# Performance work log

Hardware: AMD Instinct MI355X
Metric: run time of the kernel (lower is better)

The kernel has to match this reference:

```python
import jax, jax.numpy as jnp
import numpy as np

N = 50000          # num nodes
E = 800000         # edges per adjacency (avg degree 16)
NFEAT = 512
NHID = 256
NCLS = 100
LN_EPS = 1e-5


def spmm(rows, cols, vals, feat):
    # sparse [N,N] @ dense [N,F] via gather + segment-sum scatter
    return jax.ops.segment_sum(vals[:, None] * feat[cols], rows, num_segments=N)


def layernorm(h, g, b):
    mu = jnp.mean(h, axis=-1, keepdims=True)
    var = jnp.var(h, axis=-1, keepdims=True)
    return (h - mu) * jax.lax.rsqrt(var + LN_EPS) * g + b


def setup_inputs() -> dict:
    key = jax.random.key(0)
    ks = jax.random.split(key, 20)
    inp = {
        "x": jax.random.normal(ks[0], (N, NFEAT), dtype=jnp.float32),
        "adj_rows": jax.random.randint(ks[1], (4, E), 0, N, dtype=jnp.int32),
        "adj_cols": jax.random.randint(ks[2], (4, E), 0, N, dtype=jnp.int32),
        "adj_vals": jax.random.uniform(ks[3], (4, E), dtype=jnp.float32) / 16.0,
    }
    def lin(k, fin, fout):
        s = 1.0 / np.sqrt(fin)
        kw, kb = jax.random.split(k)
        return (jax.random.uniform(kw, (fin, fout), minval=-s, maxval=s, dtype=jnp.float32),
                jax.random.uniform(kb, (fout,), minval=-s, maxval=s, dtype=jnp.float32))
    # layer 0: GraphSage(nfeat -> nhid), LayerNorm over 2*nhid
    inp["W0"], inp["b0"] = lin(ks[4], NFEAT, NHID)
    inp["ln0_g"] = jnp.ones((2 * NHID,), jnp.float32)
    inp["ln0_b"] = jnp.zeros((2 * NHID,), jnp.float32)
    # layer 1: GCN(2*nhid -> nhid)
    inp["W1"], inp["b1"] = lin(ks[5], 2 * NHID, NHID)
    # layer 2: GraphSage(nhid -> nhid), LayerNorm over 2*nhid
    inp["W2"], inp["b2"] = lin(ks[6], NHID, NHID)
    inp["ln2_g"] = jnp.ones((2 * NHID,), jnp.float32)
    inp["ln2_b"] = jnp.zeros((2 * NHID,), jnp.float32)
    # layer 3: GCN(2*nhid -> nhid)
    inp["W3"], inp["b3"] = lin(ks[7], 2 * NHID, NHID)
    # output linear (nhid -> num_classes)
    inp["Wout"], inp["bout"] = lin(ks[8], NHID, NCLS)
    return inp


def reference(x, adj_rows, adj_cols, adj_vals,
              W0, b0, ln0_g, ln0_b, W1, b1, W2, b2, ln2_g, ln2_b, W3, b3,
              Wout, bout):
    # layer 0: GraphSage — feat = Linear(x); h = LN(concat([feat, A@feat])); ReLU; dropout(p=0)=id
    feat = x @ W0 + b0
    agg = spmm(adj_rows[0], adj_cols[0], adj_vals[0], feat)
    h = jax.nn.relu(layernorm(jnp.concatenate([feat, agg], axis=1), ln0_g, ln0_b))
    # layer 1: GCN — h = A @ Linear(h); ReLU
    h = jax.nn.relu(spmm(adj_rows[1], adj_cols[1], adj_vals[1], h @ W1 + b1))
    # layer 2: GraphSage
    feat = h @ W2 + b2
    agg = spmm(adj_rows[2], adj_cols[2], adj_vals[2], feat)
    h = jax.nn.relu(layernorm(jnp.concatenate([feat, agg], axis=1), ln2_g, ln2_b))
    # layer 3: GCN
    h = jax.nn.relu(spmm(adj_rows[3], adj_cols[3], adj_vals[3], h @ W3 + b3))
    # output head
    return h @ Wout + bout
```

## Files before the change

### kernel.cpp

```cpp
#include <hip/hip_runtime.h>

#define N_NODES 50000
#define E_EDGES 800000
#define NFEAT   512
#define NHID    256
#define NCLS    100
#define LN_EPS  1e-5f

#define NB     196
#define CHUNKA 6144
#define CAPB   6656

typedef __attribute__((ext_vector_type(8))) short bf16x8;
typedef __attribute__((ext_vector_type(4))) float f32x4;

__device__ __forceinline__ ushort bf16_rne(float x) {
    unsigned u = __float_as_uint(x);
    unsigned r = u + 0x7FFFu + ((u >> 16) & 1u);
    return (ushort)(r >> 16);
}
__device__ __forceinline__ float bf16_to_f(ushort h) {
    return __uint_as_float(((unsigned)h) << 16);
}

__device__ __forceinline__ void gload16(const void* g, void* l) {
    __builtin_amdgcn_global_load_lds(
        (const __attribute__((address_space(1))) unsigned int*)g,
        (__attribute__((address_space(3))) unsigned int*)l, 16, 0, 0);
}

__global__ __launch_bounds__(256)
void wsplit_kernel(const float* __restrict__ W, ushort* __restrict__ WT,
                   int K, int Nc, int NP)
{
    const int idx = blockIdx.x * 256 + threadIdx.x;
    if (idx >= NP * K) return;
    const int n = idx / K, k = idx - n * K;
    const float w = (n < Nc) ? W[(size_t)k * Nc + n] : 0.f;
    WT[idx] = bf16_rne(w);
}

__global__ __launch_bounds__(256)
void xconv_kernel(const float* __restrict__ x, ushort* __restrict__ xb, int n8)
{
    const int idx = blockIdx.x * 256 + threadIdx.x;
    if (idx >= n8) return;
    const float4 v0 = ((const float4*)x)[idx * 2];
    const float4 v1 = ((const float4*)x)[idx * 2 + 1];
    bf16x8 h;
    h[0] = (short)bf16_rne(v0.x); h[1] = (short)bf16_rne(v0.y);
    h[2] = (short)bf16_rne(v0.z); h[3] = (short)bf16_rne(v0.w);
    h[4] = (short)bf16_rne(v1.x); h[5] = (short)bf16_rne(v1.y);
    h[6] = (short)bf16_rne(v1.z); h[7] = (short)bf16_rne(v1.w);
    *(bf16x8*)&xb[idx * 8] = h;
}

template<int WF32, int WBF>
__global__ __launch_bounds__(512)
void gemm_mfma_bf16(const ushort* __restrict__ A1, const ushort* __restrict__ A2,
                    int K1, int K, const ushort* __restrict__ BT,
                    const float* __restrict__ bias, float* __restrict__ C,
                    ushort* __restrict__ Cbf, int M, int Nc)
{
    __shared__ __align__(16) ushort Ah[2][128 * 32];
    __shared__ __align__(16) ushort Bh[2][128 * 32];

    const int tid = threadIdx.x;
    const int bm  = blockIdx.x * 128;
    const int bn  = blockIdx.y * 128;
    const int w   = tid >> 6;
    const int l   = tid & 63;
    const int wm  = (w >> 2) * 64;
    const int wn  = (w & 3) * 32;
    const int fr  = l & 15;
    const int fq  = l >> 4;

    const int gro = l >> 2;
    const int gch = ((l & 3) ^ (gro & 3)) * 8;
    const int ldsbase = (16 * w) * 32;

    f32x4 acc[4][2];
    #pragma unroll
    for (int i = 0; i < 4; ++i) {
        acc[i][0] = (f32x4){0.f, 0.f, 0.f, 0.f};
        acc[i][1] = (f32x4){0.f, 0.f, 0.f, 0.f};
    }

    const int K2 = K - K1;
    const int NS = K / 32;

    auto stage = [&](int s, int b) {
        const int k0 = s * 32;
        gload16(&BT[(size_t)(bn + 16 * w + gro) * K + k0 + gch], &Bh[b][ldsbase]);
        const ushort* asrc;
        if (k0 < K1) asrc = &A1[(size_t)(bm + 16 * w + gro) * K1 + k0 + gch];
        else         asrc = &A2[(size_t)(bm + 16 * w + gro) * K2 + (k0 - K1) + gch];
        gload16(asrc, &Ah[b][ldsbase]);
    };

    stage(0, 0);
    __syncthreads();

    int cur = 0;
    for (int s = 0; s < NS; ++s) {
        if (s + 1 < NS) stage(s + 1, cur ^ 1);

        bf16x8 bf[2];
        #pragma unroll
        for (int nf = 0; nf < 2; ++nf) {
            const int r = wn + nf * 16 + fr;
            bf[nf] = *(const bf16x8*)&Bh[cur][r * 32 + ((fq ^ (r & 3)) * 8)];
        }
        #pragma unroll
        for (int mf = 0; mf < 4; ++mf) {
            const int r = wm + mf * 16 + fr;
            const bf16x8 af = *(const bf16x8*)&Ah[cur][r * 32 + ((fq ^ (r & 3)) * 8)];
            acc[mf][0] = __builtin_amdgcn_mfma_f32_16x16x32_bf16(af, bf[0], acc[mf][0], 0, 0, 0);
            acc[mf][1] = __builtin_amdgcn_mfma_f32_16x16x32_bf16(af, bf[1], acc[mf][1], 0, 0, 0);
        }
        __syncthreads();
        cur ^= 1;
    }

    #pragma unroll
    for (int mf = 0; mf < 4; ++mf) {
        #pragma unroll
        for (int r = 0; r < 4; ++r) {
            const int row = bm + wm + mf * 16 + fq * 4 + r;
            if (row >= M) continue;
            #pragma unroll
            for (int nf = 0; nf < 2; ++nf) {
                const int col = bn + wn + nf * 16 + fr;
                if (col < Nc) {
                    const float v = acc[mf][nf][r] + bias[col];
                    if (WF32) C[(size_t)row * Nc + col] = v;
                    if (WBF)  Cbf[(size_t)row * Nc + col] = bf16_rne(v);
                }
            }
        }
    }
}

__global__ __launch_bounds__(256)
void bin_kernel(const int* __restrict__ rows, const int* __restrict__ cols,
                const float* __restrict__ vals, int* __restrict__ bcur,
                int2* __restrict__ est)
{
    __shared__ int cnt[NB];
    __shared__ int scn[256];
    __shared__ int cstart[NB];
    __shared__ int ccur[NB];
    __shared__ int garr[NB];
    __shared__ __align__(16) int2 buf[CHUNKA];

    const int a  = blockIdx.y;
    const int e0 = blockIdx.x * CHUNKA;
    const int n  = min(CHUNKA, E_EDGES - e0);
    const int t  = threadIdx.x;
    const int*   rp = rows + (size_t)a * E_EDGES + e0;
    const int*   cp = cols + (size_t)a * E_EDGES + e0;
    const float* vp = vals + (size_t)a * E_EDGES + e0;

    if (t < NB) cnt[t] = 0;
    __syncthreads();
    for (int i = t; i < n; i += 256) atomicAdd(&cnt[((unsigned)rp[i]) >> 8], 1);
    __syncthreads();

    scn[t] = (t < NB) ? cnt[t] : 0;
    __syncthreads();
    for (int off = 1; off < 256; off <<= 1) {
        const int v = (t >= off) ? scn[t - off] : 0;
        __syncthreads();
        scn[t] += v;
        __syncthreads();
    }
    if (t < NB) {
        const int ex = scn[t] - cnt[t];
        cstart[t] = ex;
        ccur[t]   = ex;
        garr[t]   = atomicAdd(&bcur[a * NB + t], cnt[t]);
    }
    __syncthreads();

    for (int i = t; i < n; i += 256) {
        const unsigned r = (unsigned)rp[i];
        const int b = r >> 8;
        const int p = atomicAdd(&ccur[b], 1);
        buf[p] = make_int2((int)((r << 16) | (unsigned)cp[i]), __float_as_int(vp[i]));
    }
    __syncthreads();

    for (int i = t; i < n; i += 256) {
        const int2 en = buf[i];
        const int b = ((unsigned)en.x) >> 24;
        const int slot = garr[b] + (i - cstart[b]);
        if (slot < CAPB)
            est[((size_t)(a * NB + b)) * CAPB + slot] = en;
    }
}

__global__ __launch_bounds__(256)
void bscan_kernel(const int* __restrict__ bcur, int* __restrict__ bbase)
{
    __shared__ int s[256];
    const int a = blockIdx.x;
    const int t = threadIdx.x;
    const int v = (t < NB) ? bcur[a * NB + t] : 0;
    s[t] = v;
    __syncthreads();
    for (int off = 1; off < 256; off <<= 1) {
        const int u = (t >= off) ? s[t - off] : 0;
        __syncthreads();
        s[t] += u;
        __syncthreads();
    }
    if (t < NB) bbase[a * NB + t] = s[t] - v;
}

__global__ __launch_bounds__(256)
void sort_kernel(const int* __restrict__ bcur, const int* __restrict__ bbase,
                 const int2* __restrict__ est, int2* __restrict__ cpk,
                 int* __restrict__ rowstart)
{
    __shared__ __align__(16) int2 sbuf[CAPB];
    __shared__ __align__(16) int2 obuf[CAPB];
    __shared__ int cnt[256];
    __shared__ int scn[256];
    __shared__ int cur[256];

    const int a = blockIdx.y;
    const int b = blockIdx.x;
    const int t = threadIdx.x;
    const int nb = min(bcur[a * NB + b], CAPB);
    const size_t slots = ((size_t)(a * NB + b)) * CAPB;

    for (int i = t; i < nb; i += 256) sbuf[i] = est[slots + i];
    cnt[t] = 0;
    __syncthreads();
    for (int i = t; i < nb; i += 256)
        atomicAdd(&cnt[(((unsigned)sbuf[i].x) >> 16) & 255], 1);
    __syncthreads();

    scn[t] = cnt[t];
    __syncthreads();
    for (int off = 1; off < 256; off <<= 1) {
        const int v = (t >= off) ? scn[t - off] : 0;
        __syncthreads();
        scn[t] += v;
        __syncthreads();
    }
    const int excl = scn[t] - cnt[t];
    cur[t] = excl;

    const int bb = bbase[a * NB + b];
    const int r0 = b << 8;
    if (r0 + t < N_NODES)
        rowstart[(size_t)a * (N_NODES + 1) + r0 + t] = bb + excl;
    if (b == NB - 1 && t == 0)
        rowstart[(size_t)a * (N_NODES + 1) + N_NODES] = E_EDGES;
    __syncthreads();

    for (int i = t; i < nb; i += 256) {
        const int2 en = sbuf[i];
        const int r = (((unsigned)en.x) >> 16) & 255;
        const int p = atomicAdd(&cur[r], 1);
        obuf[p] = make_int2(en.x & 0xFFFF, en.y);
    }
    __syncthreads();

    int2* co = cpk + (size_t)a * E_EDGES + bb;
    for (int i = t; i < nb; i += 256) co[i] = obuf[i];
}

template<int LNFUSE>
__global__ __launch_bounds__(256)
void spmm_kernel(const int* __restrict__ rowstart, const int2* __restrict__ cpk,
                 const ushort* __restrict__ feat, ushort* __restrict__ out0,
                 ushort* __restrict__ out1, const float* __restrict__ g,
                 const float* __restrict__ be)
{
    const int row  = __builtin_amdgcn_readfirstlane((blockIdx.x * 256 + threadIdx.x) >> 6);
    const int lane = threadIdx.x & 63;

    const int s = __builtin_amdgcn_readfirstlane(rowstart[row]);
    const int e = __builtin_amdgcn_readfirstlane(rowstart[row + 1]);

    const ushort* fbase = feat + lane * 4;
    float ax = 0.f, ay = 0.f, az = 0.f, aw = 0.f;

    for (int j = s; j < e; j += 16) {
        #pragma unroll
        for (int q = 0; q < 16; ++q) {
            if (j + q < e) {
                const int2 ev = cpk[j + q];
                const float v = __int_as_float(ev.y);
                const uint2 f = *(const uint2*)(fbase + (size_t)ev.x * NHID);
                ax += v * __uint_as_float(f.x << 16);
                ay += v * __uint_as_float(f.x & 0xFFFF0000u);
                az += v * __uint_as_float(f.y << 16);
                aw += v * __uint_as_float(f.y & 0xFFFF0000u);
            }
        }
    }

    if (LNFUSE) {
        const uint2 fx = *(const uint2*)(fbase + (size_t)row * NHID);
        float xf[4] = {__uint_as_float(fx.x << 16), __uint_as_float(fx.x & 0xFFFF0000u),
                       __uint_as_float(fx.y << 16), __uint_as_float(fx.y & 0xFFFF0000u)};

        float sum = xf[0] + xf[1] + xf[2] + xf[3] + ax + ay + az + aw;
        #pragma unroll
        for (int m = 1; m < 64; m <<= 1) sum += __shfl_xor(sum, m, 64);
        const float mean = sum * (1.f / 512.f);

        float sq = 0.f;
        #pragma unroll
        for (int jj = 0; jj < 4; ++jj) { const float d = xf[jj] - mean; sq += d * d; }
        { float d; d = ax - mean; sq += d * d; d = ay - mean; sq += d * d;
          d = az - mean; sq += d * d; d = aw - mean; sq += d * d; }
        #pragma unroll
        for (int m = 1; m < 64; m <<= 1) sq += __shfl_xor(sq, m, 64);
        const float rstd = rsqrtf(sq * (1.f / 512.f) + LN_EPS);

        const int col = lane * 4;
        const float av[4] = {ax, ay, az, aw};
        ushort4 o0, o1;
        float t0[4], t1[4];
        #pragma unroll
        for (int jj = 0; jj < 4; ++jj) {
            t0[jj] = fmaxf((xf[jj] - mean) * rstd * g[col + jj] + be[col + jj], 0.f);
            t1[jj] = fmaxf((av[jj] - mean) * rstd * g[256 + col + jj] + be[256 + col + jj], 0.f);
        }
        o0.x = bf16_rne(t0[0]); o0.y = bf16_rne(t0[1]); o0.z = bf16_rne(t0[2]); o0.w = bf16_rne(t0[3]);
        o1.x = bf16_rne(t1[0]); o1.y = bf16_rne(t1[1]); o1.z = bf16_rne(t1[2]); o1.w = bf16_rne(t1[3]);
        *(ushort4*)&out0[(size_t)row * NHID + col] = o0;
        *(ushort4*)&out1[(size_t)row * NHID + col] = o1;
    } else {
        ushort4 o;
        o.x = bf16_rne(fmaxf(ax, 0.f)); o.y = bf16_rne(fmaxf(ay, 0.f));
        o.z = bf16_rne(fmaxf(az, 0.f)); o.w = bf16_rne(fmaxf(aw, 0.f));
        *(ushort4*)&out0[(size_t)row * NHID + lane * 4] = o;
    }
}

extern "C" void kernel_launch(void* const* d_in, const int* in_sizes, int n_in,
                              void* d_out, int out_size, void* d_ws, size_t ws_size,
                              hipStream_t stream)
{
    const float* x    = (const float*)d_in[0];
    const int*   rows = (const int*)  d_in[1];
    const int*   cols = (const int*)  d_in[2];
    const float* vals = (const float*)d_in[3];
    const float* W0   = (const float*)d_in[4];
    const float* b0   = (const float*)d_in[5];
    const float* g0   = (const float*)d_in[6];
    const float* be0  = (const float*)d_in[7];
    const float* W1   = (const float*)d_in[8];
    const float* b1   = (const float*)d_in[9];
    const float* W2   = (const float*)d_in[10];
    const float* b2   = (const float*)d_in[11];
    const float* g2   = (const float*)d_in[12];
    const float* be2  = (const float*)d_in[13];
    const float* W3   = (const float*)d_in[14];
    const float* b3   = (const float*)d_in[15];
    const float* Wout = (const float*)d_in[16];
    const float* bout = (const float*)d_in[17];
    float* out = (float*)d_out;

    char* wsb = (char*)d_ws;
    size_t off = 0;
    auto carve = [&](size_t bytes) { void* p = wsb + off; off += (bytes + 255) & ~(size_t)255; return p; };
    int*    rowstart = (int*)   carve((size_t)4 * (N_NODES + 1) * 4);
    int*    bcur     = (int*)   carve((size_t)4 * NB * 4);
    int*    bbase    = (int*)   carve((size_t)4 * NB * 4);
    int2*   cpk      = (int2*)  carve((size_t)4 * E_EDGES * 8);
    int2*   est      = (int2*)  carve((size_t)4 * NB * CAPB * 8);
    ushort* Xb       = (ushort*)carve((size_t)N_NODES * NFEAT * 2);
    ushort* F        = (ushort*)carve((size_t)N_NODES * NHID * 2);
    ushort* P        = (ushort*)carve((size_t)N_NODES * NHID * 2);
    ushort* Q        = (ushort*)carve((size_t)N_NODES * NHID * 2);
    ushort* G        = (ushort*)carve((size_t)N_NODES * NHID * 2);
    ushort* H        = (ushort*)carve((size_t)N_NODES * NHID * 2);
    ushort* W0T = (ushort*)carve((size_t)256 * 512 * 2);
    ushort* W1T = (ushort*)carve((size_t)256 * 512 * 2);
    ushort* W2T = (ushort*)carve((size_t)256 * 256 * 2);
    ushort* W3T = (ushort*)carve((size_t)256 * 512 * 2);
    ushort* WoT = (ushort*)carve((size_t)128 * 256 * 2);
    carve(131072);

    const dim3 blk(256);
    const dim3 blkg(512);
    const dim3 g_gemm(391, 2);
    const dim3 g_head(391, 1);
    const dim3 g_bin((E_EDGES + CHUNKA - 1) / CHUNKA, 4);
    const dim3 g_sort(NB, 4);
    const int  row_blocks = (N_NODES * 64 + 255) / 256;

    wsplit_kernel<<<(256*512 + 255)/256, blk, 0, stream>>>(W0,   W0T, 512, 256, 256);
    wsplit_kernel<<<(256*512 + 255)/256, blk, 0, stream>>>(W1,   W1T, 512, 256, 256);
    wsplit_kernel<<<(256*256 + 255)/256, blk, 0, stream>>>(W2,   W2T, 256, 256, 256);
    wsplit_kernel<<<(256*512 + 255)/256, blk, 0, stream>>>(W3,   W3T, 512, 256, 256);
    wsplit_kernel<<<(128*256 + 255)/256, blk, 0, stream>>>(Wout, WoT, 256, 100, 128);
    xconv_kernel<<<(N_NODES * NFEAT / 8 + 255)/256, blk, 0, stream>>>(x, Xb, N_NODES * NFEAT / 8);

    hipMemsetAsync(bcur, 0, (size_t)4 * NB * 4, stream);
    bin_kernel<<<g_bin, blk, 0, stream>>>(rows, cols, vals, bcur, est);
    bscan_kernel<<<4, blk, 0, stream>>>(bcur, bbase);
    sort_kernel<<<g_sort, blk, 0, stream>>>(bcur, bbase, est, cpk, rowstart);

    const int* rs0 = rowstart;
    const int* rs1 = rowstart + (N_NODES + 1);
    const int* rs2 = rowstart + 2 * (N_NODES + 1);
    const int* rs3 = rowstart + 3 * (N_NODES + 1);
    const int2* c0 = cpk;
    const int2* c1 = cpk + E_EDGES;
    const int2* c2 = cpk + 2 * (size_t)E_EDGES;
    const int2* c3 = cpk + 3 * (size_t)E_EDGES;

    gemm_mfma_bf16<0,1><<<g_gemm, blkg, 0, stream>>>(Xb, Xb, 512, 512, W0T, b0, nullptr, F, N_NODES, 256);
    spmm_kernel<1><<<row_blocks, blk, 0, stream>>>(rs0, c0, F, P, Q, g0, be0);

    gemm_mfma_bf16<0,1><<<g_gemm, blkg, 0, stream>>>(P, Q, 256, 512, W1T, b1, nullptr, G, N_NODES, 256);
    spmm_kernel<0><<<row_blocks, blk, 0, stream>>>(rs1, c1, G, H, nullptr, nullptr, nullptr);

    gemm_mfma_bf16<0,1><<<g_gemm, blkg, 0, stream>>>(H, H, 256, 256, W2T, b2, nullptr, F, N_NODES, 256);
    spmm_kernel<1><<<row_blocks, blk, 0, stream>>>(rs2, c2, F, P, Q, g2, be2);

    gemm_mfma_bf16<0,1><<<g_gemm, blkg, 0, stream>>>(P, Q, 256, 512, W3T, b3, nullptr, G, N_NODES, 256);
    spmm_kernel<0><<<row_blocks, blk, 0, stream>>>(rs3, c3, G, H, nullptr, nullptr, nullptr);

    gemm_mfma_bf16<1,0><<<g_head, blkg, 0, stream>>>(H, H, 256, 256, WoT, bout, out, nullptr, N_NODES, 100);
}
```

Before: 529.1 us.

## Merge prep kernels and memset, fold bucket scan into sort, split SpMM tail

The five weight-transpose launches, the x-to-bf16 conversion and the bucket-counter memset are merged into one prep kernel. The separate bucket prefix-scan kernel is removed; each sort block now computes its own base offset with a shared-memory reduction over the preceding bucket counts. The SpMM inner loop drops the per-edge bounds check by running full 16-edge groups unguarded, followed by a scalar remainder loop. This cuts about eight launches and some branch overhead, at the cost of redundant per-block reductions in the sort kernel.

Result: faster. 484.5 us (-8.4%).

```diff
diff --git a/kernel.cpp b/kernel.cpp
--- a/kernel.cpp
+++ b/kernel.cpp
@@ -11,6 +11,10 @@
 #define CHUNKA 6144
 #define CAPB   6656
 
+#define WT_TOTAL  (256*512 + 256*512 + 256*256 + 256*512 + 128*256)
+#define XC_TOTAL  (N_NODES * NFEAT / 8)
+#define PREP_TOTAL (WT_TOTAL + XC_TOTAL + 4 * NB)
+
 typedef __attribute__((ext_vector_type(8))) short bf16x8;
 typedef __attribute__((ext_vector_type(4))) float f32x4;
 
@@ -30,29 +34,40 @@
 }
 
 __global__ __launch_bounds__(256)
-void wsplit_kernel(const float* __restrict__ W, ushort* __restrict__ WT,
-                   int K, int Nc, int NP)
-{
-    const int idx = blockIdx.x * 256 + threadIdx.x;
-    if (idx >= NP * K) return;
-    const int n = idx / K, k = idx - n * K;
-    const float w = (n < Nc) ? W[(size_t)k * Nc + n] : 0.f;
-    WT[idx] = bf16_rne(w);
-}
-
-__global__ __launch_bounds__(256)
-void xconv_kernel(const float* __restrict__ x, ushort* __restrict__ xb, int n8)
-{
-    const int idx = blockIdx.x * 256 + threadIdx.x;
-    if (idx >= n8) return;
-    const float4 v0 = ((const float4*)x)[idx * 2];
-    const float4 v1 = ((const float4*)x)[idx * 2 + 1];
-    bf16x8 h;
-    h[0] = (short)bf16_rne(v0.x); h[1] = (short)bf16_rne(v0.y);
-    h[2] = (short)bf16_rne(v0.z); h[3] = (short)bf16_rne(v0.w);
-    h[4] = (short)bf16_rne(v1.x); h[5] = (short)bf16_rne(v1.y);
-    h[6] = (short)bf16_rne(v1.z); h[7] = (short)bf16_rne(v1.w);
-    *(bf16x8*)&xb[idx * 8] = h;
+void prep_kernel(const float* __restrict__ W0, const float* __restrict__ W1,
+                 const float* __restrict__ W2, const float* __restrict__ W3,
+                 const float* __restrict__ Wo, const float* __restrict__ x,
+                 ushort* __restrict__ W0T, ushort* __restrict__ W1T,
+                 ushort* __restrict__ W2T, ushort* __restrict__ W3T,
+                 ushort* __restrict__ WoT, ushort* __restrict__ Xb,
+                 int* __restrict__ bcur)
+{
+    int idx = blockIdx.x * 256 + threadIdx.x;
+    if (idx < WT_TOTAL) {
+        const float* W; ushort* WT; int K, Nc;
+        if      (idx < 131072) { W = W0; WT = W0T; K = 512; Nc = 256; }
+        else if (idx < 262144) { idx -= 131072; W = W1; WT = W1T; K = 512; Nc = 256; }
+        else if (idx < 327680) { idx -= 262144; W = W2; WT = W2T; K = 256; Nc = 256; }
+        else if (idx < 458752) { idx -= 327680; W = W3; WT = W3T; K = 512; Nc = 256; }
+        else                   { idx -= 458752; W = Wo; WT = WoT; K = 256; Nc = 100; }
+        const int n = idx / K, k = idx - n * K;
+        WT[idx] = bf16_rne((n < Nc) ? W[(size_t)k * Nc + n] : 0.f);
+        return;
+    }
+    idx -= WT_TOTAL;
+    if (idx < XC_TOTAL) {
+        const float4 v0 = ((const float4*)x)[idx * 2];
+        const float4 v1 = ((const float4*)x)[idx * 2 + 1];
+        bf16x8 h;
+        h[0] = (short)bf16_rne(v0.x); h[1] = (short)bf16_rne(v0.y);
+        h[2] = (short)bf16_rne(v0.z); h[3] = (short)bf16_rne(v0.w);
+        h[4] = (short)bf16_rne(v1.x); h[5] = (short)bf16_rne(v1.y);
+        h[6] = (short)bf16_rne(v1.z); h[7] = (short)bf16_rne(v1.w);
+        *(bf16x8*)&Xb[idx * 8] = h;
+        return;
+    }
+    idx -= XC_TOTAL;
+    if (idx < 4 * NB) bcur[idx] = 0;
 }
 
 template<int WF32, int WBF>
@@ -200,27 +215,8 @@
 }
 
 __global__ __launch_bounds__(256)
-void bscan_kernel(const int* __restrict__ bcur, int* __restrict__ bbase)
-{
-    __shared__ int s[256];
-    const int a = blockIdx.x;
-    const int t = threadIdx.x;
-    const int v = (t < NB) ? bcur[a * NB + t] : 0;
-    s[t] = v;
-    __syncthreads();
-    for (int off = 1; off < 256; off <<= 1) {
-        const int u = (t >= off) ? s[t - off] : 0;
-        __syncthreads();
-        s[t] += u;
-        __syncthreads();
-    }
-    if (t < NB) bbase[a * NB + t] = s[t] - v;
-}
-
-__global__ __launch_bounds__(256)
-void sort_kernel(const int* __restrict__ bcur, const int* __restrict__ bbase,
-                 const int2* __restrict__ est, int2* __restrict__ cpk,
-                 int* __restrict__ rowstart)
+void sort_kernel(const int* __restrict__ bcur, const int2* __restrict__ est,
+                 int2* __restrict__ cpk, int* __restrict__ rowstart)
 {
     __shared__ __align__(16) int2 sbuf[CAPB];
     __shared__ __align__(16) int2 obuf[CAPB];
@@ -232,9 +228,18 @@
     const int b = blockIdx.x;
     const int t = threadIdx.x;
     const int nb = min(bcur[a * NB + b], CAPB);
-    const size_t slots = ((size_t)(a * NB + b)) * CAPB;
-
-    for (int i = t; i < nb; i += 256) sbuf[i] = est[slots + i];
+    const int2* ei = est + ((size_t)(a * NB + b)) * CAPB;
+
+    scn[t] = (t < b) ? bcur[a * NB + t] : 0;
+    __syncthreads();
+    for (int o = 128; o > 0; o >>= 1) {
+        if (t < o) scn[t] += scn[t + o];
+        __syncthreads();
+    }
+    const int bb = scn[0];
+    __syncthreads();
+
+    for (int i = t; i < nb; i += 256) sbuf[i] = ei[i];
     cnt[t] = 0;
     __syncthreads();
     for (int i = t; i < nb; i += 256)
@@ -252,7 +257,6 @@
     const int excl = scn[t] - cnt[t];
     cur[t] = excl;
 
-    const int bb = bbase[a * NB + b];
     const int r0 = b << 8;
     if (r0 + t < N_NODES)
         rowstart[(size_t)a * (N_NODES + 1) + r0 + t] = bb + excl;
@@ -288,19 +292,27 @@
     const ushort* fbase = feat + lane * 4;
     float ax = 0.f, ay = 0.f, az = 0.f, aw = 0.f;
 
-    for (int j = s; j < e; j += 16) {
+    int j = s;
+    for (; j + 16 <= e; j += 16) {
         #pragma unroll
         for (int q = 0; q < 16; ++q) {
-            if (j + q < e) {
-                const int2 ev = cpk[j + q];
-                const float v = __int_as_float(ev.y);
-                const uint2 f = *(const uint2*)(fbase + (size_t)ev.x * NHID);
-                ax += v * __uint_as_float(f.x << 16);
-                ay += v * __uint_as_float(f.x & 0xFFFF0000u);
-                az += v * __uint_as_float(f.y << 16);
-                aw += v * __uint_as_float(f.y & 0xFFFF0000u);
-            }
+            const int2 ev = cpk[j + q];
+            const float v = __int_as_float(ev.y);
+            const uint2 f = *(const uint2*)(fbase + (size_t)ev.x * NHID);
+            ax += v * __uint_as_float(f.x << 16);
+            ay += v * __uint_as_float(f.x & 0xFFFF0000u);
+            az += v * __uint_as_float(f.y << 16);
+            aw += v * __uint_as_float(f.y & 0xFFFF0000u);
         }
+    }
+    for (; j < e; ++j) {
+        const int2 ev = cpk[j];
+        const float v = __int_as_float(ev.y);
+        const uint2 f = *(const uint2*)(fbase + (size_t)ev.x * NHID);
+        ax += v * __uint_as_float(f.x << 16);
+        ay += v * __uint_as_float(f.x & 0xFFFF0000u);
+        az += v * __uint_as_float(f.y << 16);
+        aw += v * __uint_as_float(f.y & 0xFFFF0000u);
     }
 
     if (LNFUSE) {
@@ -372,7 +384,6 @@
     auto carve = [&](size_t bytes) { void* p = wsb + off; off += (bytes + 255) & ~(size_t)255; return p; };
     int*    rowstart = (int*)   carve((size_t)4 * (N_NODES + 1) * 4);
     int*    bcur     = (int*)   carve((size_t)4 * NB * 4);
-    int*    bbase    = (int*)   carve((size_t)4 * NB * 4);
     int2*   cpk      = (int2*)  carve((size_t)4 * E_EDGES * 8);
     int2*   est      = (int2*)  carve((size_t)4 * NB * CAPB * 8);
     ushort* Xb       = (ushort*)carve((size_t)N_NODES * NFEAT * 2);
@@ -394,19 +405,13 @@
     const dim3 g_head(391, 1);
     const dim3 g_bin((E_EDGES + CHUNKA - 1) / CHUNKA, 4);
     const dim3 g_sort(NB, 4);
-    const int  row_blocks = (N_NODES * 64 + 255) / 256;
-
-    wsplit_kernel<<<(256*512 + 255)/256, blk, 0, stream>>>(W0,   W0T, 512, 256, 256);
-    wsplit_kernel<<<(256*512 + 255)/256, blk, 0, stream>>>(W1,   W1T, 512, 256, 256);
-    wsplit_kernel<<<(256*256 + 255)/256, blk, 0, stream>>>(W2,   W2T, 256, 256, 256);
-    wsplit_kernel<<<(256*512 + 255)/256, blk, 0, stream>>>(W3,   W3T, 512, 256, 256);
-    wsplit_kernel<<<(128*256 + 255)/256, blk, 0, stream>>>(Wout, WoT, 256, 100, 128);
-    xconv_kernel<<<(N_NODES * NFEAT / 8 + 255)/256, blk, 0, stream>>>(x, Xb, N_NODES * NFEAT / 8);
-
-    hipMemsetAsync(bcur, 0, (size_t)4 * NB * 4, stream);
+    const int  row_blocks  = (N_NODES * 64 + 255) / 256;
+    const int  prep_blocks = (PREP_TOTAL + 255) / 256;
+
+    prep_kernel<<<prep_blocks, blk, 0, stream>>>(W0, W1, W2, W3, Wout, x,
+                                                 W0T, W1T, W2T, W3T, WoT, Xb, bcur);
     bin_kernel<<<g_bin, blk, 0, stream>>>(rows, cols, vals, bcur, est);
-    bscan_kernel<<<4, blk, 0, stream>>>(bcur, bbase);
-    sort_kernel<<<g_sort, blk, 0, stream>>>(bcur, bbase, est, cpk, rowstart);
+    sort_kernel<<<g_sort, blk, 0, stream>>>(bcur, est, cpk, rowstart);
 
     const int* rs0 = rowstart;
     const int* rs1 = rowstart + (N_NODES + 1);
```
